# Kernel tuning notes

Measured on AMD Instinct MI355X. Metric: run time of the kernel, lower is better.

## Reference

```python
import jax, jax.numpy as jnp
import numpy as np

GRID = (8, 8, 8)    # grid_size
BLOCK = (4, 8, 8)   # block_size
EPS = 1e-5


def _block(x, ps):
    # x: (n,c,d,h,w) -> (n,c, gd*gh*gw, fd*fh*fw)
    n, c, d, h, w = x.shape
    gd, gh, gw = d // ps[0], h // ps[1], w // ps[2]
    x = x.reshape(n, c, gd, ps[0], gh, ps[1], gw, ps[2])
    x = x.transpose(0, 1, 2, 4, 6, 3, 5, 7)  # n,c,gd,gh,gw,fd,fh,fw
    return x.reshape(n, c, gd * gh * gw, ps[0] * ps[1] * ps[2])


def _unblock(x, gs, ps):
    # x: (n,c,G,P) -> (n,c, gd*fd, gh*fh, gw*fw)
    n, c, G, P = x.shape
    x = x.reshape(n, c, gs[0], gs[1], gs[2], ps[0], ps[1], ps[2])
    x = x.transpose(0, 1, 2, 5, 3, 6, 4, 7)
    return x.reshape(n, c, gs[0] * ps[0], gs[1] * ps[1], gs[2] * ps[2])


def setup_inputs() -> dict:
    key = jax.random.key(0)
    ks = jax.random.split(key, 9)
    c = 64
    G = GRID[0] * GRID[1] * GRID[2]    # 512
    P = BLOCK[0] * BLOCK[1] * BLOCK[2]  # 256
    x = jax.random.normal(ks[0], (4, c, 32, 64, 64), jnp.float32)
    def lin(k, fan_out, fan_in):
        s = 1.0 / np.sqrt(fan_in)
        kw, kb = jax.random.split(k)
        W = jax.random.uniform(kw, (fan_out, fan_in), jnp.float32, -s, s)
        b = jax.random.uniform(kb, (fan_out,), jnp.float32, -s, s)
        return W, b
    W1, b1 = lin(ks[1], 2 * c, c)
    W2, b2 = lin(ks[2], G, G)
    W3, b3 = lin(ks[3], P, P)
    W4, b4 = lin(ks[4], c, 2 * c)
    return {"x": x, "W1": W1, "b1": b1, "W2": W2, "b2": b2,
            "W3": W3, "b3": b3, "W4": W4, "b4": b4}


def reference(x, W1, b1, W2, b2, W3, b3, W4, b4):
    n, c, d, h, w = x.shape
    # LayerNorm over (c,d,h,w); affine params are freshly-initialized ones/zeros
    mu = x.mean(axis=(1, 2, 3, 4), keepdims=True)
    var = x.var(axis=(1, 2, 3, 4), keepdims=True)
    x = (x - mu) * jax.lax.rsqrt(var + EPS)
    # linear1 over channel dim (swapaxes+Linear+swapaxes == channel einsum)
    x = jnp.einsum('ncdhw,kc->nkdhw', x, W1) + b1[None, :, None, None, None]
    x = jax.nn.gelu(x, approximate=False)  # torch F.gelu default is exact erf
    u, v = jnp.split(x, 2, axis=1)
    # u: grid-mixing MLP over G = gd*gh*gw tokens
    gd, gh, gw = GRID
    pu = (d // gd, h // gh, w // gw)
    u = _block(u, pu)                                    # (n,c,G,Pu)
    u = jnp.einsum('ncgp,kg->nckp', u, W2) + b2[None, None, :, None]
    u = _unblock(u, GRID, pu)
    # v: block-mixing MLP over P = fd*fh*fw tokens
    fd, fh, fw = BLOCK
    gv = (d // fd, h // fh, w // fw)
    v = _block(v, BLOCK)                                 # (n,c,Gv,P)
    v = jnp.einsum('ncgp,kp->ncgk', v, W3) + b3
    v = _unblock(v, gv, BLOCK)
    x = jnp.concatenate([u, v], axis=1)                  # (n,2c,d,h,w)
    x = jnp.einsum('ncdhw,kc->nkdhw', x, W4) + b4[None, :, None, None, None]
    return x
```

## Files before the change

### kernel.cpp

```cpp
#include <hip/hip_runtime.h>
#include <hip/hip_bf16.h>
#include <math.h>


#define S_PER_N 131072
#define CNT_PER_N 8388608.0f

typedef __attribute__((ext_vector_type(8))) short bf16x8;
typedef __attribute__((ext_vector_type(4))) float f32x4;

__device__ __forceinline__ float b2f(unsigned short u) {
    return __uint_as_float(((unsigned int)u) << 16);
}
__device__ __forceinline__ unsigned short f2b(float f) {
    unsigned int i = __float_as_uint(f);
    unsigned int r = i + 0x7FFFu + ((i >> 16) & 1u);
    return (unsigned short)(r >> 16);
}
__device__ __forceinline__ unsigned int pk2(float lo, float hi) {
    unsigned int r;
    asm("v_cvt_pk_bf16_f32 %0, %1, %2" : "=v"(r) : "v"(lo), "v"(hi));
    return r;
}
__device__ __forceinline__ float loadIn(const void* p, long i, bool f32) {
    return f32 ? ((const float*)p)[i] : b2f(((const unsigned short*)p)[i]);
}
__device__ __forceinline__ void gld16(const unsigned short* g, unsigned short* l) {
    __builtin_amdgcn_global_load_lds(
        (const __attribute__((address_space(1))) void*)g,
        (__attribute__((address_space(3))) void*)l,
        16, 0, 0);
}
__device__ __forceinline__ float fast_gelu(float x) {
    const float x2 = x * x;
    const float c = -0.102944f * x2 - 2.3022081f;
    const float q = x * c;
    const float t = __builtin_amdgcn_rcpf(1.0f + __builtin_amdgcn_exp2f(q));
    return x * t;
}

__global__ void k_detect(const unsigned short* __restrict__ xw, float* __restrict__ flag) {
    __shared__ int sh[256];
    int tid = threadIdx.x;
    int sane = 0;
    for (int i = tid; i < 4096; i += 256) {
        int e = (xw[i] >> 7) & 0xFF;
        sane += (e >= 110 && e <= 130) ? 1 : 0;
    }
    sh[tid] = sane; __syncthreads();
    for (int off = 128; off; off >>= 1) {
        if (tid < off) sh[tid] += sh[tid + off];
        __syncthreads();
    }
    if (tid == 0) flag[0] = (sh[0] >= 3300) ? 0.0f : 1.0f;
}

__global__ __launch_bounds__(256) void k_stats_prepW(const void* __restrict__ xp,
                                                     const float* __restrict__ flag,
                                                     float* __restrict__ partials,
                                                     const void* __restrict__ W1,
                                                     const void* __restrict__ W2,
                                                     const void* __restrict__ W3,
                                                     const void* __restrict__ W4,
                                                     unsigned short* __restrict__ W1b,
                                                     unsigned short* __restrict__ W2b,
                                                     unsigned short* __restrict__ W3b,
                                                     unsigned short* __restrict__ W4b) {
    const bool f32 = flag[0] > 0.5f;
    if (blockIdx.x >= 512) {
        const int i = (blockIdx.x - 512) * 256 + threadIdx.x;
        if (i < 512 * 512) W2b[i] = f32 ? f2b(((const float*)W2)[i]) : ((const unsigned short*)W2)[i];
        if (i < 256 * 256) W3b[i] = f32 ? f2b(((const float*)W3)[i]) : ((const unsigned short*)W3)[i];
        if (i < 128 * 64)  W1b[i] = f32 ? f2b(((const float*)W1)[i]) : ((const unsigned short*)W1)[i];
        if (i < 64 * 128)  W4b[i] = f32 ? f2b(((const float*)W4)[i]) : ((const unsigned short*)W4)[i];
        return;
    }
    const int bid = blockIdx.x;
    const long base = (long)bid * 65536;
    float s = 0.0f, sq = 0.0f;
    if (f32) {
        const float4* xv = (const float4*)((const float*)xp + base);
        for (int it = 0; it < 64; ++it) {
            float4 v = xv[it * 256 + threadIdx.x];
            s  += v.x + v.y + v.z + v.w;
            sq += v.x*v.x + v.y*v.y + v.z*v.z + v.w*v.w;
        }
    } else {
        const uint4* xv = (const uint4*)((const unsigned short*)xp + base);
        for (int it = 0; it < 32; ++it) {
            uint4 v = xv[it * 256 + threadIdx.x];
            unsigned int ws4[4] = {v.x, v.y, v.z, v.w};
            #pragma unroll
            for (int q = 0; q < 4; ++q) {
                float f0 = b2f((unsigned short)(ws4[q] & 0xFFFFu));
                float f1 = b2f((unsigned short)(ws4[q] >> 16));
                s += f0 + f1;
                sq += f0 * f0 + f1 * f1;
            }
        }
    }
    __shared__ float ls[256], lq[256];
    ls[threadIdx.x] = s; lq[threadIdx.x] = sq;
    __syncthreads();
    for (int off = 128; off > 0; off >>= 1) {
        if (threadIdx.x < off) {
            ls[threadIdx.x] += ls[threadIdx.x + off];
            lq[threadIdx.x] += lq[threadIdx.x + off];
        }
        __syncthreads();
    }
    if (threadIdx.x == 0) {
        partials[bid * 2 + 0] = ls[0];
        partials[bid * 2 + 1] = lq[0];
    }
}

__global__ void k_red_prep(const float* __restrict__ partials, float* __restrict__ stats,
                           const void* __restrict__ W1, const void* __restrict__ b1,
                           const float* __restrict__ flag, float* __restrict__ ck) {
    const int t = threadIdx.x;
    if (t < 4) {
        float s = 0.0f, sq = 0.0f;
        for (int i = 0; i < 128; ++i) {
            s  += partials[(t * 128 + i) * 2 + 0];
            sq += partials[(t * 128 + i) * 2 + 1];
        }
        stats[t * 2 + 0] = s;
        stats[t * 2 + 1] = sq;
    }
    __syncthreads();
    const bool f32 = flag[0] > 0.5f;
    float rs = 0.0f;
    for (int c = 0; c < 64; ++c) rs += loadIn(W1, (long)t * 64 + c, f32);
    const float bb = loadIn(b1, t, f32);
    for (int n = 0; n < 4; ++n) {
        const float mu   = stats[n * 2 + 0] * (1.0f / CNT_PER_N);
        const float m2   = stats[n * 2 + 1] * (1.0f / CNT_PER_N);
        const float rstd = rsqrtf(m2 - mu * mu + 1e-5f);
        ck[n * 128 + t] = bb - rstd * mu * rs;
    }
}

__device__ __forceinline__ bf16x8 fragLd(const unsigned short* lds, int r, int c) {
    return *(const bf16x8*)&lds[r * 64 + ((c ^ (r & 7)) << 3)];
}

__global__ __launch_bounds__(256) void k_fc1_mfma(const void* __restrict__ xp,
                                                  const float* __restrict__ stats,
                                                  const float* __restrict__ ck,
                                                  const unsigned short* __restrict__ W1b,
                                                  const float* __restrict__ flag,
                                                  unsigned short* __restrict__ AuBase,
                                                  void* __restrict__ outBase, int nBase) {
    const bool f32 = flag[0] > 0.5f;
    __shared__ __align__(16) unsigned short Bs[256 * 64];
    const int nwg = gridDim.x;
    const int cpx = nwg >> 3;
    const int work = (blockIdx.x & 7) * cpx + (blockIdx.x >> 3);
    const int nl = work >> 9;
    const int n = nBase + nl;
    const int g = work & 511;
    const int d0 = (g >> 6) * 4, h0 = ((g >> 3) & 7) * 8, w0 = (g & 7) * 8;
    const int t = threadIdx.x;
    const int lane = t & 63, wid = t >> 6;
    const int waveP = wid * 64;
    const int lr = lane & 15, lk = lane >> 4;

    unsigned short* Au = AuBase + (size_t)nl * 8388608;
    unsigned short* Bv = (unsigned short*)((char*)outBase + (size_t)n * 8388608 * (f32 ? 4 : 2));

    {
        const int c0 = (t & 31) * 2;
        const int rdh = t >> 5;
        const long cbase = ((long)(n * 64 + c0)) << 17;
        const int ch = c0 >> 3, cof = c0 & 7;
        #pragma unroll
        for (int q = 0; q < 4; ++q) {
            const int dh = rdh * 4 + q;
            const int dp = dh >> 3, hp = dh & 7;
            const long sb = (long)(d0 + dp) * 4096 + (h0 + hp) * 64 + w0;
            const int pbase = dp * 64 + hp * 8;
            if (f32) {
                const float* r0 = (const float*)xp + cbase + sb;
                const float* r1 = r0 + S_PER_N;
                float4 a0 = *(const float4*)r0, a1 = *(const float4*)(r0 + 4);
                float4 b0 = *(const float4*)r1, b1v = *(const float4*)(r1 + 4);
                float ff0[8] = {a0.x, a0.y, a0.z, a0.w, a1.x, a1.y, a1.z, a1.w};
                float ff1[8] = {b0.x, b0.y, b0.z, b0.w, b1v.x, b1v.y, b1v.z, b1v.w};
                #pragma unroll
                for (int j = 0; j < 8; ++j) {
                    const int pj = pbase + j;
                    *(unsigned int*)&Bs[pj * 64 + ((ch ^ (pj & 7)) << 3) + cof] = pk2(ff0[j], ff1[j]);
                }
            } else {
                const unsigned short* r0 = (const unsigned short*)xp + cbase + sb;
                uint4 a = *(const uint4*)r0;
                uint4 b = *(const uint4*)(r0 + S_PER_N);
                const unsigned short* pa = (const unsigned short*)&a;
                const unsigned short* pb = (const unsigned short*)&b;
                #pragma unroll
                for (int j = 0; j < 8; ++j) {
                    const int pj = pbase + j;
                    unsigned int val = (unsigned int)pa[j] | ((unsigned int)pb[j] << 16);
                    *(unsigned int*)&Bs[pj * 64 + ((ch ^ (pj & 7)) << 3) + cof] = val;
                }
            }
        }
    }
    __syncthreads();

    const float mu   = stats[n * 2 + 0] * (1.0f / CNT_PER_N);
    const float m2   = stats[n * 2 + 1] * (1.0f / CNT_PER_N);
    const float rstd = rsqrtf(m2 - mu * mu + 1e-5f);

    #pragma unroll
    for (int half = 0; half < 2; ++half) {
        f32x4 zero = {0.f, 0.f, 0.f, 0.f};
        f32x4 acc[4][4];
        #pragma unroll
        for (int i = 0; i < 4; ++i)
            #pragma unroll
            for (int j = 0; j < 4; ++j) acc[i][j] = zero;

        #pragma unroll
        for (int kk = 0; kk < 2; ++kk) {
            bf16x8 bp[4], aj[4];
            #pragma unroll
            for (int f = 0; f < 4; ++f) {
                bp[f] = fragLd(Bs, waveP + f * 16 + lr, kk * 4 + lk);
                aj[f] = *(const bf16x8*)(W1b + (long)(half * 64 + f * 16 + lr) * 64 + (kk * 4 + lk) * 8);
            }
            #pragma unroll
            for (int fp = 0; fp < 4; ++fp)
                #pragma unroll
                for (int fj = 0; fj < 4; ++fj)
                    acc[fp][fj] = __builtin_amdgcn_mfma_f32_16x16x32_bf16(bp[fp], aj[fj], acc[fp][fj], 0, 0, 0);
        }

        #pragma unroll
        for (int fj = 0; fj < 4; ++fj) {
            const int j = half * 64 + fj * 16 + lr;
            const float ckj = ck[n * 128 + j];
            #pragma unroll
            for (int fp = 0; fp < 4; ++fp) {
                const int pb = waveP + fp * 16 + lk * 4;
                float gg[4];
                #pragma unroll
                for (int i = 0; i < 4; ++i)
                    gg[i] = fast_gelu(acc[fp][fj][i] * rstd + ckj);
                uint2 pk;
                pk.x = pk2(gg[0], gg[1]);
                pk.y = pk2(gg[2], gg[3]);
                if (half == 0) {
                    *(uint2*)&Au[(long)j * S_PER_N + g * 256 + pb] = pk;
                } else {
                    *(uint2*)&Bv[((long)g * 64 + (j - 64)) * 256 + pb] = pk;
                }
            }
        }
    }
}

__global__ __launch_bounds__(256) void k_tv(const unsigned short* __restrict__ AuBase,
                                            void* __restrict__ outBase,
                                            const unsigned short* __restrict__ W3b,
                                            const void* __restrict__ b3,
                                            const float* __restrict__ flag,
                                            unsigned short* __restrict__ AtBase,
                                            unsigned short* __restrict__ TVBase,
                                            int nBase, int nV) {
    __shared__ __align__(16) unsigned short smem[17408];
    const int t = threadIdx.x;

    if ((int)blockIdx.x < nV) {
        const bool f32 = flag[0] > 0.5f;
        unsigned short* As = smem;
        unsigned short* Bs = smem + 8192;
        unsigned short* Ot = smem;
        const int bid = blockIdx.x;
        const int nl = bid >> 9;
        const int n = nBase + nl;
        const int inner = bid & 511;
        const unsigned short* Bv = (const unsigned short*)((char*)outBase + (size_t)n * 8388608 * (f32 ? 4 : 2));
        unsigned short* TV = TVBase + (size_t)nl * 8388608;
        const int mTile = inner >> 8;
        const int nTile = inner & 255;
        const int m0 = mTile * 128;
        const int lane = t & 63, wid = t >> 6;
        const int waveM = (wid >> 1) * 64, waveN = (wid & 1) * 64;
        const int lr = lane & 15, lk = lane >> 4;
        const int rIn8 = lane >> 3;
        const int swzOff = ((lane & 7) ^ rIn8) << 3;

        f32x4 zero = {0.f, 0.f, 0.f, 0.f};
        f32x4 acc[4][4];
        #pragma unroll
        for (int i = 0; i < 4; ++i)
            #pragma unroll
            for (int j = 0; j < 4; ++j) acc[i][j] = zero;

        for (int kb = 0; kb < 256; kb += 64) {
            #pragma unroll
            for (int call = 0; call < 4; ++call) {
                const int rowBase = call * 32 + wid * 8;
                gld16(W3b + (long)(m0 + rowBase + rIn8) * 256 + kb + swzOff, As + rowBase * 64);
                gld16(Bv + (long)(nTile * 128 + rowBase + rIn8) * 256 + kb + swzOff, Bs + rowBase * 64);
            }
            __syncthreads();
            #pragma unroll
            for (int kk = 0; kk < 2; ++kk) {
                bf16x8 tok[4], wf[4];
                #pragma unroll
                for (int f = 0; f < 4; ++f) {
                    tok[f] = fragLd(Bs, waveN + f * 16 + lr, kk * 4 + lk);
                    wf[f]  = fragLd(As, waveM + f * 16 + lr, kk * 4 + lk);
                }
                #pragma unroll
                for (int fm = 0; fm < 4; ++fm)
                    #pragma unroll
                    for (int fn = 0; fn < 4; ++fn)
                        acc[fm][fn] = __builtin_amdgcn_mfma_f32_16x16x32_bf16(tok[fm], wf[fn], acc[fm][fn], 0, 0, 0);
            }
            __syncthreads();
        }

        #pragma unroll
        for (int fn = 0; fn < 4; ++fn) {
            const int kp = waveM + fn * 16 + lr;
            const float bias = loadIn(b3, m0 + kp, f32);
            #pragma unroll
            for (int fm = 0; fm < 4; ++fm) {
                const int nb = waveN + fm * 16 + lk * 4;
                uint2 pk;
                pk.x = pk2(acc[fm][fn][0] + bias, acc[fm][fn][1] + bias);
                pk.y = pk2(acc[fm][fn][2] + bias, acc[fm][fn][3] + bias);
                *(uint2*)&Ot[kp * 136 + nb] = pk;
            }
        }
        __syncthreads();
        {
            const int m = t >> 1, half = t & 1;
            const unsigned short* src = &Ot[m * 136 + half * 64];
            unsigned short* dst = TV + ((long)(nTile * 2 + half) * 256 + m0 + m) * 64;
            #pragma unroll
            for (int q = 0; q < 8; ++q)
                *(uint4*)(dst + q * 8) = *(const uint4*)(src + q * 8);
        }
    } else {
        unsigned short* T = smem;
        const int bid = blockIdx.x - nV;
        const int nl = bid >> 11;
        const int inner = bid & 2047;
        const unsigned short* A = AuBase + (size_t)nl * 8388608;
        unsigned short* At = AtBase + (size_t)nl * 8388608;
        const int c  = inner >> 5;
        const int gt = (inner >> 2) & 7, pt = inner & 3;
        const int g0 = gt * 64, p0 = pt * 64;

        const int gr = t >> 2, pc = (t & 3) * 16;
        const unsigned int* s32 = (const unsigned int*)(A + (long)c * S_PER_N + (long)(g0 + gr) * 256 + p0 + pc);
        unsigned int* d32 = (unsigned int*)&T[gr * 66 + pc];
        #pragma unroll
        for (int i = 0; i < 8; ++i) d32[i] = s32[i];
        __syncthreads();

        const int pr = t >> 2, gc0 = (t & 3) * 16;
        unsigned int ov[8];
        #pragma unroll
        for (int i = 0; i < 8; ++i) {
            unsigned int lo = T[(gc0 + 2 * i) * 66 + pr];
            unsigned int hi = T[(gc0 + 2 * i + 1) * 66 + pr];
            ov[i] = lo | (hi << 16);
        }
        unsigned int* dst = (unsigned int*)(At + ((long)(p0 + pr) * 64 + c) * 512 + g0 + gc0);
        #pragma unroll
        for (int i = 0; i < 8; ++i) dst[i] = ov[i];
    }
}

__global__ __launch_bounds__(256) void k_umix_mfma(const unsigned short* __restrict__ BtBase,
                                                   const unsigned short* __restrict__ W2b,
                                                   const void* __restrict__ b2,
                                                   const float* __restrict__ flag,
                                                   unsigned short* __restrict__ TUBase) {
    const bool f32 = flag[0] > 0.5f;
    __shared__ __align__(16) unsigned short smem[17408];
    unsigned short* As = smem;
    unsigned short* Bs = smem + 8192;
    unsigned short* Ot = smem;
    const int bid = blockIdx.x;
    const int nl = bid >> 9;
    const int inner = bid & 511;
    const unsigned short* Bt = BtBase + (size_t)nl * 8388608;
    unsigned short* TU = TUBase + (size_t)nl * 8388608;
    const int mTile = inner >> 7;
    const int nTile = inner & 127;
    const int m0 = mTile * 128;
    const int t = threadIdx.x;
    const int lane = t & 63, wid = t >> 6;
    const int waveM = (wid >> 1) * 64, waveN = (wid & 1) * 64;
    const int lr = lane & 15, lk = lane >> 4;
    const int rIn8 = lane >> 3;
    const int swzOff = ((lane & 7) ^ rIn8) << 3;

    f32x4 zero = {0.f, 0.f, 0.f, 0.f};
    f32x4 acc[4][4];
    #pragma unroll
    for (int i = 0; i < 4; ++i)
        #pragma unroll
        for (int j = 0; j < 4; ++j) acc[i][j] = zero;

    for (int kb = 0; kb < 512; kb += 64) {
        #pragma unroll
        for (int call = 0; call < 4; ++call) {
            const int rowBase = call * 32 + wid * 8;
            gld16(W2b + (long)(m0 + rowBase + rIn8) * 512 + kb + swzOff, As + rowBase * 64);
            gld16(Bt + (long)(nTile * 128 + rowBase + rIn8) * 512 + kb + swzOff, Bs + rowBase * 64);
        }
        __syncthreads();
        #pragma unroll
        for (int kk = 0; kk < 2; ++kk) {
            bf16x8 tok[4], wf[4];
            #pragma unroll
            for (int f = 0; f < 4; ++f) {
                tok[f] = fragLd(Bs, waveN + f * 16 + lr, kk * 4 + lk);
                wf[f]  = fragLd(As, waveM + f * 16 + lr, kk * 4 + lk);
            }
            #pragma unroll
            for (int fm = 0; fm < 4; ++fm)
                #pragma unroll
                for (int fn = 0; fn < 4; ++fn)
                    acc[fm][fn] = __builtin_amdgcn_mfma_f32_16x16x32_bf16(tok[fm], wf[fn], acc[fm][fn], 0, 0, 0);
        }
        __syncthreads();
    }

    #pragma unroll
    for (int fn = 0; fn < 4; ++fn) {
        const int gp = waveM + fn * 16 + lr;
        const float bias = loadIn(b2, m0 + gp, f32);
        #pragma unroll
        for (int fm = 0; fm < 4; ++fm) {
            const int nb = waveN + fm * 16 + lk * 4;
            uint2 pk;
            pk.x = pk2(acc[fm][fn][0] + bias, acc[fm][fn][1] + bias);
            pk.y = pk2(acc[fm][fn][2] + bias, acc[fm][fn][3] + bias);
            *(uint2*)&Ot[gp * 136 + nb] = pk;
        }
    }
    __syncthreads();
    {
        const int m = t >> 1, half = t & 1;
        const unsigned short* src = &Ot[m * 136 + half * 64];
        unsigned short* dst = TU + ((long)(m0 + m) * 256 + nTile * 2 + half) * 64;
        #pragma unroll
        for (int q = 0; q < 8; ++q)
            *(uint4*)(dst + q * 8) = *(const uint4*)(src + q * 8);
    }
}

__global__ __launch_bounds__(256) void k_fc2_mfma(const unsigned short* __restrict__ TUBase,
                                                  const unsigned short* __restrict__ TVBase,
                                                  const unsigned short* __restrict__ W4b,
                                                  const void* __restrict__ b4,
                                                  const float* __restrict__ flag,
                                                  void* __restrict__ out, int nBase) {
    const bool f32 = flag[0] > 0.5f;
    const int bid = blockIdx.x;
    const int nl = bid >> 10;
    const int n = nBase + nl;
    const unsigned short* TU = TUBase + (size_t)nl * 8388608;
    const unsigned short* TV = TVBase + (size_t)nl * 8388608;
    const int s0 = (bid & 1023) * 128;
    const int t = threadIdx.x;
    const int lane = t & 63, wid = t >> 6;
    const int lr = lane & 15, lk = lane >> 4;
    const int tokBase = s0 + wid * 32;

    long gpv[2];
    #pragma unroll
    for (int ft = 0; ft < 2; ++ft) {
        const int s = tokBase + ft * 16 + lr;
        const int d = s >> 12, h = (s >> 6) & 63, w = s & 63;
        const int g = ((d >> 2) << 6) | ((h >> 3) << 3) | (w >> 3);
        const int p = ((d & 3) << 6) | ((h & 7) << 3) | (w & 7);
        gpv[ft] = (long)g * 256 + p;
    }

    f32x4 zero = {0.f, 0.f, 0.f, 0.f};
    f32x4 acc[2][4];
    #pragma unroll
    for (int i = 0; i < 2; ++i)
        #pragma unroll
        for (int j = 0; j < 4; ++j) acc[i][j] = zero;

    #pragma unroll
    for (int kk = 0; kk < 4; ++kk) {
        const unsigned short* base = (kk < 2) ? TU : TV;
        const int choff = ((kk & 1) * 4 + lk) * 8;
        bf16x8 ta[2], wb[4];
        #pragma unroll
        for (int ft = 0; ft < 2; ++ft)
            ta[ft] = *(const bf16x8*)(base + gpv[ft] * 64 + choff);
        #pragma unroll
        for (int fk = 0; fk < 4; ++fk)
            wb[fk] = *(const bf16x8*)(W4b + (long)(fk * 16 + lr) * 128 + (kk * 4 + lk) * 8);
        #pragma unroll
        for (int ft = 0; ft < 2; ++ft)
            #pragma unroll
            for (int fk = 0; fk < 4; ++fk)
                acc[ft][fk] = __builtin_amdgcn_mfma_f32_16x16x32_bf16(ta[ft], wb[fk], acc[ft][fk], 0, 0, 0);
    }

    float bias[4];
    #pragma unroll
    for (int fk = 0; fk < 4; ++fk) bias[fk] = loadIn(b4, fk * 16 + lr, f32);

    #pragma unroll
    for (int ft = 0; ft < 2; ++ft) {
        const int tok0 = tokBase + ft * 16 + lk * 4;
        #pragma unroll
        for (int fk = 0; fk < 4; ++fk) {
            const int k = fk * 16 + lr;
            const long off = ((long)(n * 64 + k) << 17) + tok0;
            if (f32) {
                float4 v = {acc[ft][fk][0] + bias[fk], acc[ft][fk][1] + bias[fk],
                            acc[ft][fk][2] + bias[fk], acc[ft][fk][3] + bias[fk]};
                *(float4*)((float*)out + off) = v;
            } else {
                uint2 pk;
                pk.x = pk2(acc[ft][fk][0] + bias[fk], acc[ft][fk][1] + bias[fk]);
                pk.y = pk2(acc[ft][fk][2] + bias[fk], acc[ft][fk][3] + bias[fk]);
                *(uint2*)((unsigned short*)out + off) = pk;
            }
        }
    }
}

extern "C" void kernel_launch(void* const* d_in, const int* in_sizes, int n_in,
                              void* d_out, int out_size, void* d_ws, size_t ws_size,
                              hipStream_t stream) {
    const void* x  = d_in[0];
    const void* W1 = d_in[1];
    const void* b1 = d_in[2];
    const void* W2 = d_in[3];
    const void* b2 = d_in[4];
    const void* W3 = d_in[5];
    const void* b3 = d_in[6];
    const void* W4 = d_in[7];
    const void* b4 = d_in[8];

    float* wsf      = (float*)d_ws;
    float* stats    = wsf;
    float* flag     = wsf + 8;
    float* partials = wsf + 16;
    float* ck       = wsf + 1040;

    unsigned short* W2bf = (unsigned short*)((char*)d_ws + 8192);
    unsigned short* W3bf = W2bf + 512 * 512;
    unsigned short* W1bf = W3bf + 256 * 256;
    unsigned short* W4bf = W1bf + 128 * 64;

    const size_t perBuf = (size_t)8388608;
    const size_t need4  = (1u << 20) + 3ull * 4ull * perBuf * 2ull;
    const int cnt = (ws_size >= need4) ? 4 : 1;

    unsigned short* buf1 = (unsigned short*)((char*)d_ws + (1u << 20));
    unsigned short* buf2 = buf1 + (size_t)cnt * perBuf;
    unsigned short* buf3 = buf2 + (size_t)cnt * perBuf;

    hipLaunchKernelGGL(k_detect,      dim3(1),    dim3(256), 0, stream,
                       (const unsigned short*)x, flag);
    hipLaunchKernelGGL(k_stats_prepW, dim3(1536), dim3(256), 0, stream,
                       x, flag, partials, W1, W2, W3, W4, W1bf, W2bf, W3bf, W4bf);
    hipLaunchKernelGGL(k_red_prep,    dim3(1),    dim3(128), 0, stream,
                       partials, stats, W1, b1, flag, ck);

    for (int nBase = 0; nBase < 4; nBase += cnt) {
        hipLaunchKernelGGL(k_fc1_mfma,  dim3(cnt * 512),  dim3(256), 0, stream,
                           x, stats, ck, W1bf, flag, buf2, d_out, nBase);
        hipLaunchKernelGGL(k_tv,        dim3(cnt * 2560), dim3(256), 0, stream,
                           buf2, d_out, W3bf, b3, flag, buf1, buf3, nBase, cnt * 512);
        hipLaunchKernelGGL(k_umix_mfma, dim3(cnt * 512),  dim3(256), 0, stream,
                           buf1, W2bf, b2, flag, buf2);
        hipLaunchKernelGGL(k_fc2_mfma,  dim3(cnt * 1024), dim3(256), 0, stream,
                           buf2, buf3, W4bf, b4, flag, d_out, nBase);
    }
}
```

Baseline: 333.8 us.

## Fuse block-mixing W3 GEMM into fc1 kernel, keeping v half in LDS

The fc1 kernel now keeps the GELU'd v half of each grid block in shared memory and applies the W3 block-mixing GEMM plus bias right away, writing TV directly. This removes the v round trip through global memory (previously staged in the output buffer) and the separate k_tv GEMM pass. The u half is also staged through LDS so its stores are coalesced 16-byte writes, and its transpose moves into a standalone k_transA kernel. LDS use per workgroup roughly doubles (two 32KB buffers), which lowers occupancy, and the fc1 kernel now carries more serialized work.

```diff
diff --git a/kernel.cpp b/kernel.cpp
--- a/kernel.cpp
+++ b/kernel.cpp
@@ -145,15 +145,19 @@
     return *(const bf16x8*)&lds[r * 64 + ((c ^ (r & 7)) << 3)];
 }
 
-__global__ __launch_bounds__(256) void k_fc1_mfma(const void* __restrict__ xp,
-                                                  const float* __restrict__ stats,
-                                                  const float* __restrict__ ck,
-                                                  const unsigned short* __restrict__ W1b,
-                                                  const float* __restrict__ flag,
-                                                  unsigned short* __restrict__ AuBase,
-                                                  void* __restrict__ outBase, int nBase) {
+__global__ __launch_bounds__(256) void k_fc1v(const void* __restrict__ xp,
+                                              const float* __restrict__ stats,
+                                              const float* __restrict__ ck,
+                                              const unsigned short* __restrict__ W1b,
+                                              const unsigned short* __restrict__ W3b,
+                                              const void* __restrict__ b3,
+                                              const float* __restrict__ flag,
+                                              unsigned short* __restrict__ AuBase,
+                                              unsigned short* __restrict__ TVBase,
+                                              int nBase) {
     const bool f32 = flag[0] > 0.5f;
-    __shared__ __align__(16) unsigned short Bs[256 * 64];
+    __shared__ __align__(16) unsigned short Xs[256 * 64];
+    __shared__ __align__(16) unsigned short R2[64 * 256];
     const int nwg = gridDim.x;
     const int cpx = nwg >> 3;
     const int work = (blockIdx.x & 7) * cpx + (blockIdx.x >> 3);
@@ -167,7 +171,7 @@
     const int lr = lane & 15, lk = lane >> 4;
 
     unsigned short* Au = AuBase + (size_t)nl * 8388608;
-    unsigned short* Bv = (unsigned short*)((char*)outBase + (size_t)n * 8388608 * (f32 ? 4 : 2));
+    unsigned short* TVg = TVBase + (size_t)nl * 8388608 + (long)g * 16384;
 
     {
         const int c0 = (t & 31) * 2;
@@ -190,7 +194,7 @@
                 #pragma unroll
                 for (int j = 0; j < 8; ++j) {
                     const int pj = pbase + j;
-                    *(unsigned int*)&Bs[pj * 64 + ((ch ^ (pj & 7)) << 3) + cof] = pk2(ff0[j], ff1[j]);
+                    *(unsigned int*)&Xs[pj * 64 + ((ch ^ (pj & 7)) << 3) + cof] = pk2(ff0[j], ff1[j]);
                 }
             } else {
                 const unsigned short* r0 = (const unsigned short*)xp + cbase + sb;
@@ -202,7 +206,7 @@
                 for (int j = 0; j < 8; ++j) {
                     const int pj = pbase + j;
                     unsigned int val = (unsigned int)pa[j] | ((unsigned int)pb[j] << 16);
-                    *(unsigned int*)&Bs[pj * 64 + ((ch ^ (pj & 7)) << 3) + cof] = val;
+                    *(unsigned int*)&Xs[pj * 64 + ((ch ^ (pj & 7)) << 3) + cof] = val;
                 }
             }
         }
@@ -213,22 +217,20 @@
     const float m2   = stats[n * 2 + 1] * (1.0f / CNT_PER_N);
     const float rstd = rsqrtf(m2 - mu * mu + 1e-5f);
 
-    #pragma unroll
-    for (int half = 0; half < 2; ++half) {
+    {
         f32x4 zero = {0.f, 0.f, 0.f, 0.f};
         f32x4 acc[4][4];
         #pragma unroll
         for (int i = 0; i < 4; ++i)
             #pragma unroll
             for (int j = 0; j < 4; ++j) acc[i][j] = zero;
-
         #pragma unroll
         for (int kk = 0; kk < 2; ++kk) {
             bf16x8 bp[4], aj[4];
             #pragma unroll
             for (int f = 0; f < 4; ++f) {
-                bp[f] = fragLd(Bs, waveP + f * 16 + lr, kk * 4 + lk);
-                aj[f] = *(const bf16x8*)(W1b + (long)(half * 64 + f * 16 + lr) * 64 + (kk * 4 + lk) * 8);
+                bp[f] = fragLd(Xs, waveP + f * 16 + lr, kk * 4 + lk);
+                aj[f] = *(const bf16x8*)(W1b + (long)(f * 16 + lr) * 64 + (kk * 4 + lk) * 8);
             }
             #pragma unroll
             for (int fp = 0; fp < 4; ++fp)
@@ -236,146 +238,166 @@
                 for (int fj = 0; fj < 4; ++fj)
                     acc[fp][fj] = __builtin_amdgcn_mfma_f32_16x16x32_bf16(bp[fp], aj[fj], acc[fp][fj], 0, 0, 0);
         }
-
         #pragma unroll
         for (int fj = 0; fj < 4; ++fj) {
-            const int j = half * 64 + fj * 16 + lr;
-            const float ckj = ck[n * 128 + j];
+            const int c = fj * 16 + lr;
+            const float ckj = ck[n * 128 + c];
             #pragma unroll
             for (int fp = 0; fp < 4; ++fp) {
                 const int pb = waveP + fp * 16 + lk * 4;
-                float gg[4];
-                #pragma unroll
-                for (int i = 0; i < 4; ++i)
-                    gg[i] = fast_gelu(acc[fp][fj][i] * rstd + ckj);
+                float g0v = fast_gelu(acc[fp][fj][0] * rstd + ckj);
+                float g1v = fast_gelu(acc[fp][fj][1] * rstd + ckj);
+                float g2v = fast_gelu(acc[fp][fj][2] * rstd + ckj);
+                float g3v = fast_gelu(acc[fp][fj][3] * rstd + ckj);
                 uint2 pk;
-                pk.x = pk2(gg[0], gg[1]);
-                pk.y = pk2(gg[2], gg[3]);
-                if (half == 0) {
-                    *(uint2*)&Au[(long)j * S_PER_N + g * 256 + pb] = pk;
-                } else {
-                    *(uint2*)&Bv[((long)g * 64 + (j - 64)) * 256 + pb] = pk;
-                }
-            }
-        }
-    }
-}
-
-__global__ __launch_bounds__(256) void k_tv(const unsigned short* __restrict__ AuBase,
-                                            void* __restrict__ outBase,
-                                            const unsigned short* __restrict__ W3b,
-                                            const void* __restrict__ b3,
-                                            const float* __restrict__ flag,
-                                            unsigned short* __restrict__ AtBase,
-                                            unsigned short* __restrict__ TVBase,
-                                            int nBase, int nV) {
-    __shared__ __align__(16) unsigned short smem[17408];
-    const int t = threadIdx.x;
-
-    if ((int)blockIdx.x < nV) {
-        const bool f32 = flag[0] > 0.5f;
-        unsigned short* As = smem;
-        unsigned short* Bs = smem + 8192;
-        unsigned short* Ot = smem;
-        const int bid = blockIdx.x;
-        const int nl = bid >> 9;
-        const int n = nBase + nl;
-        const int inner = bid & 511;
-        const unsigned short* Bv = (const unsigned short*)((char*)outBase + (size_t)n * 8388608 * (f32 ? 4 : 2));
-        unsigned short* TV = TVBase + (size_t)nl * 8388608;
-        const int mTile = inner >> 8;
-        const int nTile = inner & 255;
-        const int m0 = mTile * 128;
-        const int lane = t & 63, wid = t >> 6;
-        const int waveM = (wid >> 1) * 64, waveN = (wid & 1) * 64;
-        const int lr = lane & 15, lk = lane >> 4;
-        const int rIn8 = lane >> 3;
-        const int swzOff = ((lane & 7) ^ rIn8) << 3;
-
+                pk.x = pk2(g0v, g1v);
+                pk.y = pk2(g2v, g3v);
+                *(uint2*)&R2[c * 256 + (((pb >> 3) ^ (c & 7)) << 3) + (pb & 7)] = pk;
+            }
+        }
+    }
+    __syncthreads();
+    uint4 aud[8];
+    {
+        const int c2 = t >> 2, part = t & 3;
+        #pragma unroll
+        for (int q = 0; q < 8; ++q)
+            aud[q] = *(const uint4*)&R2[c2 * 256 + ((part * 8 + (q ^ (c2 & 7))) << 3)];
+    }
+    __syncthreads();
+    {
+        const int c2 = t >> 2, part = t & 3;
+        unsigned short* dst = Au + (long)c2 * S_PER_N + g * 256 + part * 64;
+        #pragma unroll
+        for (int q = 0; q < 8; ++q)
+            *(uint4*)(dst + q * 8) = aud[q];
+    }
+
+    {
         f32x4 zero = {0.f, 0.f, 0.f, 0.f};
         f32x4 acc[4][4];
         #pragma unroll
         for (int i = 0; i < 4; ++i)
             #pragma unroll
             for (int j = 0; j < 4; ++j) acc[i][j] = zero;
-
+        #pragma unroll
+        for (int kk = 0; kk < 2; ++kk) {
+            bf16x8 bp[4], aj[4];
+            #pragma unroll
+            for (int f = 0; f < 4; ++f) {
+                bp[f] = fragLd(Xs, waveP + f * 16 + lr, kk * 4 + lk);
+                aj[f] = *(const bf16x8*)(W1b + (long)(64 + f * 16 + lr) * 64 + (kk * 4 + lk) * 8);
+            }
+            #pragma unroll
+            for (int fp = 0; fp < 4; ++fp)
+                #pragma unroll
+                for (int fj = 0; fj < 4; ++fj)
+                    acc[fp][fj] = __builtin_amdgcn_mfma_f32_16x16x32_bf16(bp[fp], aj[fj], acc[fp][fj], 0, 0, 0);
+        }
+        #pragma unroll
+        for (int fj = 0; fj < 4; ++fj) {
+            const int c = fj * 16 + lr;
+            const float ckj = ck[n * 128 + 64 + c];
+            #pragma unroll
+            for (int fp = 0; fp < 4; ++fp) {
+                const int pb = waveP + fp * 16 + lk * 4;
+                float g0v = fast_gelu(acc[fp][fj][0] * rstd + ckj);
+                float g1v = fast_gelu(acc[fp][fj][1] * rstd + ckj);
+                float g2v = fast_gelu(acc[fp][fj][2] * rstd + ckj);
+                float g3v = fast_gelu(acc[fp][fj][3] * rstd + ckj);
+                uint2 pk;
+                pk.x = pk2(g0v, g1v);
+                pk.y = pk2(g2v, g3v);
+                *(uint2*)&R2[c * 256 + (((pb >> 3) ^ (c & 7)) << 3) + (pb & 7)] = pk;
+            }
+        }
+    }
+    __syncthreads();
+
+    {
+        const int wk = wid * 64;
+        f32x4 zero = {0.f, 0.f, 0.f, 0.f};
+        f32x4 acc2[4][4];
+        #pragma unroll
+        for (int i = 0; i < 4; ++i)
+            #pragma unroll
+            for (int j = 0; j < 4; ++j) acc2[i][j] = zero;
+        #pragma unroll
+        for (int kk = 0; kk < 8; ++kk) {
+            bf16x8 am[4], wf[4];
+            #pragma unroll
+            for (int f = 0; f < 4; ++f) {
+                const int cr = f * 16 + lr;
+                am[f] = *(const bf16x8*)&R2[cr * 256 + (((kk * 4 + lk) ^ (cr & 7)) << 3)];
+                wf[f] = *(const bf16x8*)(W3b + (long)(wk + f * 16 + lr) * 256 + (kk * 4 + lk) * 8);
+            }
+            #pragma unroll
+            for (int fc = 0; fc < 4; ++fc)
+                #pragma unroll
+                for (int fk = 0; fk < 4; ++fk)
+                    acc2[fc][fk] = __builtin_amdgcn_mfma_f32_16x16x32_bf16(am[fc], wf[fk], acc2[fc][fk], 0, 0, 0);
+        }
+        #pragma unroll
+        for (int fk = 0; fk < 4; ++fk) {
+            const int k = wk + fk * 16 + lr;
+            const float bias = loadIn(b3, k, f32);
+            #pragma unroll
+            for (int fc = 0; fc < 4; ++fc) {
+                const int c0 = fc * 16 + lk * 4;
+                uint2 pk;
+                pk.x = pk2(acc2[fc][fk][0] + bias, acc2[fc][fk][1] + bias);
+                pk.y = pk2(acc2[fc][fk][2] + bias, acc2[fc][fk][3] + bias);
+                *(uint2*)&Xs[k * 64 + (((c0 >> 3) ^ (k & 7)) << 3) + (c0 & 7)] = pk;
+            }
+        }
+    }
+    __syncthreads();
+
+    {
+        const int part = t & 3;
+        #pragma unroll
         for (int kb = 0; kb < 256; kb += 64) {
-            #pragma unroll
-            for (int call = 0; call < 4; ++call) {
-                const int rowBase = call * 32 + wid * 8;
-                gld16(W3b + (long)(m0 + rowBase + rIn8) * 256 + kb + swzOff, As + rowBase * 64);
-                gld16(Bv + (long)(nTile * 128 + rowBase + rIn8) * 256 + kb + swzOff, Bs + rowBase * 64);
-            }
-            __syncthreads();
-            #pragma unroll
-            for (int kk = 0; kk < 2; ++kk) {
-                bf16x8 tok[4], wf[4];
-                #pragma unroll
-                for (int f = 0; f < 4; ++f) {
-                    tok[f] = fragLd(Bs, waveN + f * 16 + lr, kk * 4 + lk);
-                    wf[f]  = fragLd(As, waveM + f * 16 + lr, kk * 4 + lk);
-                }
-                #pragma unroll
-                for (int fm = 0; fm < 4; ++fm)
-                    #pragma unroll
-                    for (int fn = 0; fn < 4; ++fn)
-                        acc[fm][fn] = __builtin_amdgcn_mfma_f32_16x16x32_bf16(tok[fm], wf[fn], acc[fm][fn], 0, 0, 0);
-            }
-            __syncthreads();
-        }
-
-        #pragma unroll
-        for (int fn = 0; fn < 4; ++fn) {
-            const int kp = waveM + fn * 16 + lr;
-            const float bias = loadIn(b3, m0 + kp, f32);
-            #pragma unroll
-            for (int fm = 0; fm < 4; ++fm) {
-                const int nb = waveN + fm * 16 + lk * 4;
-                uint2 pk;
-                pk.x = pk2(acc[fm][fn][0] + bias, acc[fm][fn][1] + bias);
-                pk.y = pk2(acc[fm][fn][2] + bias, acc[fm][fn][3] + bias);
-                *(uint2*)&Ot[kp * 136 + nb] = pk;
-            }
-        }
-        __syncthreads();
-        {
-            const int m = t >> 1, half = t & 1;
-            const unsigned short* src = &Ot[m * 136 + half * 64];
-            unsigned short* dst = TV + ((long)(nTile * 2 + half) * 256 + m0 + m) * 64;
-            #pragma unroll
-            for (int q = 0; q < 8; ++q)
-                *(uint4*)(dst + q * 8) = *(const uint4*)(src + q * 8);
-        }
-    } else {
-        unsigned short* T = smem;
-        const int bid = blockIdx.x - nV;
-        const int nl = bid >> 11;
-        const int inner = bid & 2047;
-        const unsigned short* A = AuBase + (size_t)nl * 8388608;
-        unsigned short* At = AtBase + (size_t)nl * 8388608;
-        const int c  = inner >> 5;
-        const int gt = (inner >> 2) & 7, pt = inner & 3;
-        const int g0 = gt * 64, p0 = pt * 64;
-
-        const int gr = t >> 2, pc = (t & 3) * 16;
-        const unsigned int* s32 = (const unsigned int*)(A + (long)c * S_PER_N + (long)(g0 + gr) * 256 + p0 + pc);
-        unsigned int* d32 = (unsigned int*)&T[gr * 66 + pc];
-        #pragma unroll
-        for (int i = 0; i < 8; ++i) d32[i] = s32[i];
-        __syncthreads();
-
-        const int pr = t >> 2, gc0 = (t & 3) * 16;
-        unsigned int ov[8];
-        #pragma unroll
-        for (int i = 0; i < 8; ++i) {
-            unsigned int lo = T[(gc0 + 2 * i) * 66 + pr];
-            unsigned int hi = T[(gc0 + 2 * i + 1) * 66 + pr];
-            ov[i] = lo | (hi << 16);
-        }
-        unsigned int* dst = (unsigned int*)(At + ((long)(p0 + pr) * 64 + c) * 512 + g0 + gc0);
-        #pragma unroll
-        for (int i = 0; i < 8; ++i) dst[i] = ov[i];
-    }
+            const int k = kb + (t >> 2);
+            #pragma unroll
+            for (int q = 0; q < 2; ++q) {
+                uint4 v = *(const uint4*)&Xs[k * 64 + (((part * 2 + q) ^ (k & 7)) << 3)];
+                *(uint4*)(TVg + k * 64 + part * 16 + q * 8) = v;
+            }
+        }
+    }
+}
+
+__global__ __launch_bounds__(256) void k_transA(const unsigned short* __restrict__ Abase,
+                                                unsigned short* __restrict__ AtBase) {
+    __shared__ unsigned short T[64 * 66];
+    const int bid = blockIdx.x;
+    const int nl = bid >> 11;
+    const int inner = bid & 2047;
+    const unsigned short* A = Abase + (size_t)nl * 8388608;
+    unsigned short* At = AtBase + (size_t)nl * 8388608;
+    const int c  = inner >> 5;
+    const int gt = (inner >> 2) & 7, pt = inner & 3;
+    const int g0 = gt * 64, p0 = pt * 64;
+    const int t = threadIdx.x;
+
+    const int gr = t >> 2, pc = (t & 3) * 16;
+    const unsigned int* s32 = (const unsigned int*)(A + (long)c * S_PER_N + (long)(g0 + gr) * 256 + p0 + pc);
+    unsigned int* d32 = (unsigned int*)&T[gr * 66 + pc];
+    #pragma unroll
+    for (int i = 0; i < 8; ++i) d32[i] = s32[i];
+    __syncthreads();
+
+    const int pr = t >> 2, gc0 = (t & 3) * 16;
+    unsigned int ov[8];
+    #pragma unroll
+    for (int i = 0; i < 8; ++i) {
+        unsigned int lo = T[(gc0 + 2 * i) * 66 + pr];
+        unsigned int hi = T[(gc0 + 2 * i + 1) * 66 + pr];
+        ov[i] = lo | (hi << 16);
+    }
+    unsigned int* dst = (unsigned int*)(At + ((long)(p0 + pr) * 64 + c) * 512 + g0 + gc0);
+    #pragma unroll
+    for (int i = 0; i < 8; ++i) dst[i] = ov[i];
 }
 
 __global__ __launch_bounds__(256) void k_umix_mfma(const unsigned short* __restrict__ BtBase,
@@ -577,10 +599,9 @@
                        partials, stats, W1, b1, flag, ck);
 
     for (int nBase = 0; nBase < 4; nBase += cnt) {
-        hipLaunchKernelGGL(k_fc1_mfma,  dim3(cnt * 512),  dim3(256), 0, stream,
-                           x, stats, ck, W1bf, flag, buf2, d_out, nBase);
-        hipLaunchKernelGGL(k_tv,        dim3(cnt * 2560), dim3(256), 0, stream,
-                           buf2, d_out, W3bf, b3, flag, buf1, buf3, nBase, cnt * 512);
+        hipLaunchKernelGGL(k_fc1v,      dim3(cnt * 512),  dim3(256), 0, stream,
+                           x, stats, ck, W1bf, W3bf, b3, flag, buf2, buf3, nBase);
+        hipLaunchKernelGGL(k_transA,    dim3(cnt * 2048), dim3(256), 0, stream, buf2, buf1);
         hipLaunchKernelGGL(k_umix_mfma, dim3(cnt * 512),  dim3(256), 0, stream,
                            buf1, W2bf, b2, flag, buf2);
         hipLaunchKernelGGL(k_fc2_mfma,  dim3(cnt * 1024), dim3(256), 0, stream,
```

Result: slower. 351.6 us (+5.4%).
